# Optimization experiments

Measured on AMD Instinct MI355X. Metric: run time of the kernel, lower is better.

Reference implementation:

```python
import jax, jax.numpy as jnp
import numpy as np

B, S, D, H = 4, 2048, 2048, 16
HD = D // H  # 128
THETA = 10000.0


def setup_inputs() -> dict:
    key = jax.random.key(0)
    k1, k2, k3 = jax.random.split(key, 3)
    x = jax.random.normal(k1, (B, S, D), dtype=jnp.float32)
    wqkv = jax.random.normal(k2, (3 * D, D), dtype=jnp.float32) * (1.0 / np.sqrt(D))
    wo = jax.random.normal(k3, (D, D), dtype=jnp.float32) * (1.0 / np.sqrt(D))
    return {"x": x, "wqkv": wqkv, "wo": wo}


def _rotate_half(t):
    t1 = t[..., : t.shape[-1] // 2]
    t2 = t[..., t.shape[-1] // 2 :]
    return jnp.concatenate([-t2, t1], axis=-1)


def reference(x, wqkv, wo):
    b, s, d = x.shape
    h, hd = H, HD
    # fused QKV projection (Linear without bias: x @ W^T)
    qkv = jnp.einsum("bsd,ed->bse", x, wqkv).reshape(b, s, 3, h, hd)
    xq, xk, xv = qkv[:, :, 0], qkv[:, :, 1], qkv[:, :, 2]

    # RoPE tables (start_pos = 0)
    inv_freq = 1.0 / (THETA ** (jnp.arange(0, hd, 2, dtype=jnp.float32) / hd))
    t = jnp.arange(s, dtype=jnp.float32)
    freqs = jnp.outer(t, inv_freq)  # [s, hd/2]
    cos = jnp.concatenate([jnp.cos(freqs)] * 2, axis=-1).reshape(1, s, 1, hd)
    sin = jnp.concatenate([jnp.sin(freqs)] * 2, axis=-1).reshape(1, s, 1, hd)

    xq = xq * cos + _rotate_half(xq) * sin
    xk = xk * cos + _rotate_half(xk) * sin

    # causal SDPA (kv_cache is None, seq_len > 1)
    scale = 1.0 / np.sqrt(hd)
    scores = jnp.einsum("bqhd,bkhd->bhqk", xq, xk) * scale
    causal = jnp.tril(jnp.ones((s, s), dtype=bool))
    scores = jnp.where(causal, scores, jnp.finfo(scores.dtype).min)
    attn = jax.nn.softmax(scores, axis=-1)
    out = jnp.einsum("bhqk,bkhd->bqhd", attn, xv).reshape(b, s, d)
    return jnp.einsum("bsd,od->bso", out, wo)
```

## Files before the change

### kernel.cpp

```cpp
#include <hip/hip_runtime.h>

typedef unsigned short u16;
typedef unsigned int u32;
typedef __bf16 bf16x8 __attribute__((ext_vector_type(8)));
typedef float f32x4 __attribute__((ext_vector_type(4)));

#define S_LEN 2048
#define NH 16
#define HD 128

#define AS1 __attribute__((address_space(1)))
#define AS3 __attribute__((address_space(3)))

__device__ __forceinline__ u16 f2bf(float x) {
  u32 u = __builtin_bit_cast(u32, x);
  u32 r = u + 0x7FFFu + ((u >> 16) & 1u);
  return (u16)(r >> 16);
}
__device__ __forceinline__ float bf2f(u16 b) {
  return __builtin_bit_cast(float, (u32)b << 16);
}

__global__ void cvt_f32_bf16(const float* __restrict__ in, u16* __restrict__ out, int n4) {
  int i = blockIdx.x * 256 + threadIdx.x;
  if (i >= n4) return;
  float4 v = ((const float4*)in)[i];
  ushort4 o;
  o.x = f2bf(v.x); o.y = f2bf(v.y); o.z = f2bf(v.z); o.w = f2bf(v.w);
  ((ushort4*)out)[i] = o;
}

__global__ void build_tab(float* __restrict__ tab) {
  int t = blockIdx.x * 256 + threadIdx.x;
  int s = t >> 6, j = t & 63;
  float inv = exp2f(-(float)j * 0.20762050593045083f);
  float ang = (float)s * inv;
  tab[t] = cosf(ang);
  tab[131072 + t] = sinf(ang);
}

__device__ __forceinline__ void storeC(u16* p, float v) { *p = f2bf(v); }
__device__ __forceinline__ void storeC(float* p, float v) { *p = v; }

template <typename OutT>
__global__ __launch_bounds__(512, 2) void gemm_bt6(const u16* __restrict__ A, const u16* __restrict__ B,
                                                   OutT* __restrict__ C, int M, int N, int K, int nbx) {
  __shared__ alignas(16) u16 LDS[65536];
  char* lds = (char*)LDS;
  const int tid = threadIdx.x;
  const int lane = tid & 63;
  const int w = tid >> 6;
  const int wr = w >> 2, wc = w & 3;
  const int g = lane >> 4, c = lane & 15;

  const int nwg = gridDim.x;
  const int id = blockIdx.x;
  const int sw = (id & 7) * (nwg >> 3) + (id >> 3);
  const int bx = sw % nbx, by = sw / nbx;
  const size_t rowBase = (size_t)by * 256;
  const size_t colBase = (size_t)bx * 256;

  const int half = w & 1;
  const int sub = (w >> 1) & 3;
  const size_t ldb = (size_t)K * 2;
  const int srow = lane >> 3;
  const int soff = ((lane & 7) ^ srow) << 4;
  const char* ApS = (const char*)A + (rowBase + half * 128 + srow) * ldb + soff;
  const char* BpS = (const char*)B + (colBase + half * 128 + srow) * ldb + soff;

  auto stA = [&](int u, int blk) {
    const int r0 = blk * 32 + sub * 8;
    const int dst = ((u & 1) * 2 + half) * 16384 + r0 * 128;
    __builtin_amdgcn_global_load_lds((const AS1 void*)(ApS + (size_t)r0 * ldb + (size_t)u * 128),
                                     (AS3 void*)(lds + dst), 16, 0, 0);
  };
  auto stB = [&](int u, int jj) {
    const int r0 = (sub * 4 + jj) * 8;
    const int dst = 65536 + ((u & 1) * 2 + half) * 16384 + r0 * 128;
    __builtin_amdgcn_global_load_lds((const AS1 void*)(BpS + (size_t)r0 * ldb + (size_t)u * 128),
                                     (AS3 void*)(lds + dst), 16, 0, 0);
  };

  const int swz = (c & 7) << 4;
  auto rdA = [&](int bA, int mi, int kk) -> bf16x8 {
    return *(const bf16x8*)(lds + bA + mi * 2048 + c * 128 + ((kk * 64 + g * 16) ^ swz));
  };
  auto rdB = [&](int bB, int n, int kk) -> bf16x8 {
    return *(const bf16x8*)(lds + bB + n * 2048 + c * 128 + ((kk * 64 + g * 16) ^ swz));
  };

  f32x4 acc[8][4];
#pragma unroll
  for (int m = 0; m < 8; ++m)
#pragma unroll
    for (int n = 0; n < 4; ++n) acc[m][n] = f32x4{0.f, 0.f, 0.f, 0.f};

  bf16x8 bf_[4][2];
  bf16x8 aP[4], aQ[4];

  auto loadA = [&](bf16x8 (&s)[4], int bA, int mi) {
    s[0] = rdA(bA, mi, 0); s[1] = rdA(bA, mi, 1);
    s[2] = rdA(bA, mi + 1, 0); s[3] = rdA(bA, mi + 1, 1);
  };
  auto loadR1 = [&](int bA, int bB) {
    loadA(aP, bA, 0);
#pragma unroll
    for (int n = 0; n < 4; ++n) { bf_[n][0] = rdB(bB, n, 0); bf_[n][1] = rdB(bB, n, 1); }
  };
  auto MFMA2 = [&](int mi, bf16x8 (&s)[4]) {
#pragma unroll
    for (int n = 0; n < 4; ++n) {
      acc[mi][n]     = __builtin_amdgcn_mfma_f32_16x16x32_bf16(s[0], bf_[n][0], acc[mi][n], 0, 0, 0);
      acc[mi][n]     = __builtin_amdgcn_mfma_f32_16x16x32_bf16(s[1], bf_[n][1], acc[mi][n], 0, 0, 0);
      acc[mi + 1][n] = __builtin_amdgcn_mfma_f32_16x16x32_bf16(s[2], bf_[n][0], acc[mi + 1][n], 0, 0, 0);
      acc[mi + 1][n] = __builtin_amdgcn_mfma_f32_16x16x32_bf16(s[3], bf_[n][1], acc[mi + 1][n], 0, 0, 0);
    }
  };

  const int NT = K >> 6;

#pragma unroll
  for (int b = 0; b < 4; ++b) stA(0, b);
#pragma unroll
  for (int j = 0; j < 4; ++j) stB(0, j);
#pragma unroll
  for (int b = 0; b < 4; ++b) stA(1, b);
#pragma unroll
  for (int j = 0; j < 4; ++j) stB(1, j);
  asm volatile("s_waitcnt vmcnt(8)" ::: "memory");
  __builtin_amdgcn_s_barrier();
  {
    const int bA0 = wr * 16384;
    const int bB0 = 65536 + (wc >> 1) * 16384 + (wc & 1) * 8192;
    loadR1(bA0, bB0);
  }

#pragma unroll 1
  for (int t = 0; t < NT; ++t) {
    const int bA = (t & 1) * 32768 + wr * 16384;
    const int bB = 65536 + (t & 1) * 32768 + (wc >> 1) * 16384 + (wc & 1) * 8192;
    loadA(aQ, bA, 2);
    if (t >= 1 && t + 1 < NT) stA(t + 1, 3);
    asm volatile("s_waitcnt lgkmcnt(4)" ::: "memory");
    __builtin_amdgcn_sched_barrier(0);
    __builtin_amdgcn_s_setprio(1);
    MFMA2(0, aP);
    __builtin_amdgcn_s_setprio(0);
    __builtin_amdgcn_sched_barrier(0);
    __builtin_amdgcn_s_barrier();
    loadA(aP, bA, 4);
    if (t + 2 < NT) { stA(t + 2, 0); stB(t + 2, 0); stB(t + 2, 1); }
    asm volatile("s_waitcnt lgkmcnt(4)" ::: "memory");
    __builtin_amdgcn_sched_barrier(0);
    __builtin_amdgcn_s_setprio(1);
    MFMA2(2, aQ);
    __builtin_amdgcn_s_setprio(0);
    __builtin_amdgcn_sched_barrier(0);
    __builtin_amdgcn_s_barrier();
    loadA(aQ, bA, 6);
    if (t + 2 < NT) { stA(t + 2, 1); stB(t + 2, 2); stB(t + 2, 3); }
    asm volatile("s_waitcnt lgkmcnt(4)" ::: "memory");
    __builtin_amdgcn_sched_barrier(0);
    __builtin_amdgcn_s_setprio(1);
    MFMA2(4, aP);
    __builtin_amdgcn_s_setprio(0);
    __builtin_amdgcn_sched_barrier(0);
    __builtin_amdgcn_s_barrier();
    if (t + 2 < NT) stA(t + 2, 2);
    asm volatile("s_waitcnt lgkmcnt(0)" ::: "memory");
    __builtin_amdgcn_sched_barrier(0);
    __builtin_amdgcn_s_setprio(1);
    MFMA2(6, aQ);
    __builtin_amdgcn_s_setprio(0);
    __builtin_amdgcn_sched_barrier(0);
    if (t + 2 < NT) { asm volatile("s_waitcnt vmcnt(7)" ::: "memory"); }
    else            { asm volatile("s_waitcnt vmcnt(0)" ::: "memory"); }
    __builtin_amdgcn_s_barrier();
    if (t + 1 < NT) {
      const int bA1 = ((t + 1) & 1) * 32768 + wr * 16384;
      const int bB1 = 65536 + ((t + 1) & 1) * 32768 + (wc >> 1) * 16384 + (wc & 1) * 8192;
      loadR1(bA1, bB1);
    }
  }

#pragma unroll
  for (int m = 0; m < 8; ++m)
#pragma unroll
    for (int n = 0; n < 4; ++n) {
      size_t row = rowBase + wr * 128 + m * 16 + g * 4;
      size_t col = colBase + wc * 64 + n * 16 + c;
#pragma unroll
      for (int r = 0; r < 4; ++r)
        storeC(&C[(row + r) * (size_t)N + col], acc[m][n][r]);
    }
}

__global__ void rope_qk(const u16* __restrict__ qkv, const float* __restrict__ tab,
                        u16* __restrict__ Q, u16* __restrict__ K) {
  int idx = blockIdx.x * 256 + threadIdx.x;
  int j = idx & 63;
  int s = (idx >> 6) & (S_LEN - 1);
  int h = (idx >> 17) & (NH - 1);
  int b = idx >> 21;
  float cs = tab[s * 64 + j];
  float sn = tab[131072 + s * 64 + j];
  size_t qbase = (((size_t)(b * S_LEN + s) * 3 + 0) * NH + h) * HD;
  size_t kbase = qbase + (size_t)NH * HD;
  size_t o = ((size_t)(b * NH + h) * S_LEN + s) * HD;
  float q1 = bf2f(qkv[qbase + j]),  q2 = bf2f(qkv[qbase + j + 64]);
  Q[o + j]      = f2bf(q1 * cs - q2 * sn);
  Q[o + j + 64] = f2bf(q2 * cs + q1 * sn);
  float k1 = bf2f(qkv[kbase + j]), k2 = bf2f(qkv[kbase + j + 64]);
  K[o + j]      = f2bf(k1 * cs - k2 * sn);
  K[o + j + 64] = f2bf(k2 * cs + k1 * sn);
}

__global__ void v_transpose(const u16* __restrict__ qkv, u16* __restrict__ Vt) {
  __shared__ u16 t[32][33];
  int bh = blockIdx.z;
  int s0 = blockIdx.x * 32;
  int d0 = blockIdx.y * 32;
  int b = bh >> 4, h = bh & 15;
  int col = threadIdx.x & 31;
  int row = threadIdx.x >> 5;
#pragma unroll
  for (int i = 0; i < 4; ++i) {
    int s = row + i * 8;
    t[s][col] = qkv[(((size_t)(b * S_LEN + s0 + s) * 3 + 2) * NH + h) * HD + d0 + col];
  }
  __syncthreads();
  size_t vb = ((size_t)bh * HD + d0) * S_LEN + s0;
#pragma unroll
  for (int i = 0; i < 4; ++i) {
    int d = row + i * 8;
    Vt[vb + (size_t)d * S_LEN + col] = t[col][d];
  }
}

__global__ __launch_bounds__(512, 4) void attn_fwd(const u16* __restrict__ Q, const u16* __restrict__ K,
                                                   const u16* __restrict__ Vt, u16* __restrict__ O) {
  __shared__ alignas(16) u16 Ks[2 * 64 * 128];
  __shared__ alignas(16) u16 Vs[2 * 128 * 64];
  __shared__ alignas(16) u16 Pl[8 * 16 * 64];
  const int tid = threadIdx.x;
  const int lane = tid & 63;
  const int w = tid >> 6;
  const int g = lane >> 4, c = lane & 15;
  const int bh = blockIdx.x;
  const int pair = blockIdx.y;
  const int b = bh >> 4, h = bh & 15;

  const u16* Qb = Q + (size_t)bh * S_LEN * HD;
  const u16* Kb = K + (size_t)bh * S_LEN * HD;
  const u16* Vb = Vt + (size_t)bh * HD * S_LEN;
  const float SL = 0.12751753f;
  const int swz = (c & 7) << 4;

  int ldsOff[2], srcK[2], srcV[2];
#pragma unroll
  for (int ii = 0; ii < 2; ++ii) {
    int p = (w * 2 + ii) * 1024 + lane * 16;
    ldsOff[ii] = p;
    int rk = p >> 8, ik = p & 255;
    srcK[ii] = rk * 256 + (ik ^ ((rk & 7) << 4));
    int rv = p >> 7, iv = p & 127;
    srcV[ii] = rv * (S_LEN * 2) + (iv ^ ((rv & 7) << 4));
  }
  int koff[4], voff[2];
#pragma unroll
  for (int kb = 0; kb < 4; ++kb) koff[kb] = (kb * 64 + g * 16) ^ swz;
  voff[0] = (g * 16) ^ swz;
  voff[1] = (64 + g * 16) ^ swz;
  int poff[4];
#pragma unroll
  for (int t = 0; t < 4; ++t) poff[t] = (t * 32 + g * 8) ^ swz;
  char* Pw = (char*)Pl + w * 2048;

#pragma unroll 1
  for (int ph = 0; ph < 2; ++ph) {
    const int sti = ph ? (15 - pair) : pair;
    const int qb0 = sti * 128;
    const int q0 = qb0 + w * 16;

    bf16x8 qf[4];
#pragma unroll
    for (int kb = 0; kb < 4; ++kb)
      qf[kb] = *(const bf16x8*)&Qb[(size_t)(q0 + c) * HD + kb * 32 + g * 8];

    f32x4 acc[8];
#pragma unroll
    for (int cb = 0; cb < 8; ++cb) acc[cb] = f32x4{0.f, 0.f, 0.f, 0.f};
    float m_i = -3e38f, l_i = 0.f;

    const int nsteps = sti * 2 + 2;
#pragma unroll
    for (int ii = 0; ii < 2; ++ii) {
      __builtin_amdgcn_global_load_lds((const AS1 void*)((const char*)Kb + srcK[ii]),
                                       (AS3 void*)((char*)Ks + ldsOff[ii] - lane * 16), 16, 0, 0);
      __builtin_amdgcn_global_load_lds((const AS1 void*)((const char*)Vb + srcV[ii]),
                                       (AS3 void*)((char*)Vs + ldsOff[ii] - lane * 16), 16, 0, 0);
    }
    __syncthreads();
    int cur = 0;

#pragma unroll 1
    for (int st = 0; st < nsteps; ++st) {
      const int kv0 = st << 6;
      if (st + 1 < nsteps) {
        const char* kbase = (const char*)Kb + (size_t)(kv0 + 64) * 256;
        const char* vbase = (const char*)Vb + (size_t)(kv0 + 64) * 2;
        const int nb = (cur ^ 1) * 16384;
#pragma unroll
        for (int ii = 0; ii < 2; ++ii) {
          __builtin_amdgcn_global_load_lds((const AS1 void*)(kbase + srcK[ii]),
                                           (AS3 void*)((char*)Ks + nb + ldsOff[ii] - lane * 16), 16, 0, 0);
          __builtin_amdgcn_global_load_lds((const AS1 void*)(vbase + srcV[ii]),
                                           (AS3 void*)((char*)Vs + nb + ldsOff[ii] - lane * 16), 16, 0, 0);
        }
      }
      if (kv0 < q0 + 16) {
        const char* Kt = (const char*)Ks + cur * 16384;
        const char* Vtl = (const char*)Vs + cur * 16384;
        f32x4 s[4];
#pragma unroll
        for (int t = 0; t < 4; ++t) s[t] = f32x4{0.f, 0.f, 0.f, 0.f};
#pragma unroll
        for (int t = 0; t < 4; ++t)
#pragma unroll
          for (int kb = 0; kb < 4; ++kb) {
            bf16x8 kf = *(const bf16x8*)(Kt + t * 4096 + c * 256 + koff[kb]);
            s[t] = __builtin_amdgcn_mfma_f32_16x16x32_bf16(kf, qf[kb], s[t], 0, 0, 0);
          }
        if (kv0 + 63 > q0) {
          const int lim = q0 + c - kv0 - 4 * g;
#pragma unroll
          for (int t = 0; t < 4; ++t)
#pragma unroll
            for (int r = 0; r < 4; ++r)
              s[t][r] = (16 * t + r <= lim) ? s[t][r] : -3e38f;
        }
        float mx = s[0][0];
#pragma unroll
        for (int t = 0; t < 4; ++t)
#pragma unroll
          for (int r = 0; r < 4; ++r) mx = fmaxf(mx, s[t][r]);
        mx = fmaxf(mx, __shfl_xor(mx, 16));
        mx = fmaxf(mx, __shfl_xor(mx, 32));
        const float mn = fmaxf(m_i, mx);
        const float alpha = exp2f((m_i - mn) * SL);
        float rs = 0.f;
#pragma unroll
        for (int t = 0; t < 4; ++t) {
          float p0 = exp2f((s[t][0] - mn) * SL);
          float p1 = exp2f((s[t][1] - mn) * SL);
          float p2 = exp2f((s[t][2] - mn) * SL);
          float p3 = exp2f((s[t][3] - mn) * SL);
          rs += (p0 + p1) + (p2 + p3);
          ushort4 pw;
          pw.x = f2bf(p0); pw.y = f2bf(p1); pw.z = f2bf(p2); pw.w = f2bf(p3);
          *(ushort4*)(Pw + c * 128 + poff[t]) = pw;
        }
        rs += __shfl_xor(rs, 16);
        rs += __shfl_xor(rs, 32);
        l_i = l_i * alpha + rs;
        m_i = mn;
        float ar[4];
#pragma unroll
        for (int r = 0; r < 4; ++r) ar[r] = __shfl(alpha, 4 * g + r);
#pragma unroll
        for (int cb = 0; cb < 8; ++cb)
#pragma unroll
          for (int r = 0; r < 4; ++r) acc[cb][r] *= ar[r];
        bf16x8 pa0 = *(const bf16x8*)(Pw + c * 128 + voff[0]);
        bf16x8 pa1 = *(const bf16x8*)(Pw + c * 128 + voff[1]);
#pragma unroll
        for (int cb = 0; cb < 8; ++cb) {
          bf16x8 vf0 = *(const bf16x8*)(Vtl + cb * 2048 + c * 128 + voff[0]);
          acc[cb] = __builtin_amdgcn_mfma_f32_16x16x32_bf16(pa0, vf0, acc[cb], 0, 0, 0);
          bf16x8 vf1 = *(const bf16x8*)(Vtl + cb * 2048 + c * 128 + voff[1]);
          acc[cb] = __builtin_amdgcn_mfma_f32_16x16x32_bf16(pa1, vf1, acc[cb], 0, 0, 0);
        }
      }
      __syncthreads();
      cur ^= 1;
    }
    float linv = 1.0f / l_i;
    float lr[4];
#pragma unroll
    for (int r = 0; r < 4; ++r) lr[r] = __shfl(linv, 4 * g + r);
#pragma unroll
    for (int cb = 0; cb < 8; ++cb)
#pragma unroll
      for (int r = 0; r < 4; ++r) {
        int q = q0 + 4 * g + r;
        O[(((size_t)b * S_LEN + q) * NH + h) * HD + cb * 16 + c] = f2bf(acc[cb][r] * lr[r]);
      }
  }
}

extern "C" void kernel_launch(void* const* d_in, const int* in_sizes, int n_in,
                              void* d_out, int out_size, void* d_ws, size_t ws_size,
                              hipStream_t stream) {
  const float* x    = (const float*)d_in[0];
  const float* wqkv = (const float*)d_in[1];
  const float* wo   = (const float*)d_in[2];
  float* out = (float*)d_out;
  char* ws = (char*)d_ws;

  u16*  xb    = (u16*)(ws + 0);
  u16*  wqkvb = (u16*)(ws + 33554432);
  float* tab  = (float*)(ws + 58720256);
  u16*  wob   = (u16*)(ws + 58720256);
  u16*  qkvb  = (u16*)(ws + 67108864);
  u16*  Vt    = (u16*)(ws + 167772160);
  u16*  attn  = (u16*)(ws + 0);
  u16*  Qr = (u16*)d_out;
  u16*  Kr = (u16*)d_out + 16777216;

  cvt_f32_bf16<<<16384, 256, 0, stream>>>(x, xb, 16777216 / 4);
  cvt_f32_bf16<<<12288, 256, 0, stream>>>(wqkv, wqkvb, 12582912 / 4);
  build_tab<<<512, 256, 0, stream>>>(tab);

  gemm_bt6<u16><<<768, 512, 0, stream>>>(xb, wqkvb, qkvb, 8192, 6144, 2048, 24);

  rope_qk<<<32768, 256, 0, stream>>>(qkvb, tab, Qr, Kr);
  v_transpose<<<dim3(64, 4, 64), 256, 0, stream>>>(qkvb, Vt);

  cvt_f32_bf16<<<4096, 256, 0, stream>>>(wo, wob, 4194304 / 4);

  attn_fwd<<<dim3(64, 8), 512, 0, stream>>>(Qr, Kr, Vt, attn);

  gemm_bt6<float><<<256, 512, 0, stream>>>(attn, wob, out, 8192, 2048, 2048, 8);
}
```

Measured before the change: 434.2 us.

## Fuse RoPE and V transpose into the QKV GEMM epilogue

The QKV projection GEMM now writes its outputs directly. For Q and K tiles it applies RoPE in registers and writes to head-major buffers. For V tiles it transposes through LDS and writes Vt. This removes the bf16 qkv intermediate and the separate rope_qk and v_transpose kernels, along with their global memory round trips. To make it work, the B-operand row mapping changes so each wave holds matching d and d+64 columns. The cost is a heavier epilogue with scattered 2-byte stores for Q and K and extra table loads.

```diff
diff --git a/kernel.cpp b/kernel.cpp
--- a/kernel.cpp
+++ b/kernel.cpp
@@ -3,6 +3,7 @@
 typedef unsigned short u16;
 typedef unsigned int u32;
 typedef __bf16 bf16x8 __attribute__((ext_vector_type(8)));
+typedef unsigned short u16x8 __attribute__((ext_vector_type(8)));
 typedef float f32x4 __attribute__((ext_vector_type(4)));
 
 #define S_LEN 2048
@@ -42,9 +43,12 @@
 __device__ __forceinline__ void storeC(u16* p, float v) { *p = f2bf(v); }
 __device__ __forceinline__ void storeC(float* p, float v) { *p = v; }
 
-template <typename OutT>
-__global__ __launch_bounds__(512, 2) void gemm_bt6(const u16* __restrict__ A, const u16* __restrict__ B,
-                                                   OutT* __restrict__ C, int M, int N, int K, int nbx) {
+template <int EPI, typename OutT>
+__global__ __launch_bounds__(512, 2) void gemm_fused(const u16* __restrict__ A, const u16* __restrict__ B,
+                                                     OutT* __restrict__ C, const float* __restrict__ tab,
+                                                     u16* __restrict__ Qr, u16* __restrict__ Kr,
+                                                     u16* __restrict__ Vt,
+                                                     int M, int N, int K, int nbx) {
   __shared__ alignas(16) u16 LDS[65536];
   char* lds = (char*)LDS;
   const int tid = threadIdx.x;
@@ -81,12 +85,16 @@
                                      (AS3 void*)(lds + dst), 16, 0, 0);
   };
 
+  const int dq32 = (wc & 1) * 32;
   const int swz = (c & 7) << 4;
   auto rdA = [&](int bA, int mi, int kk) -> bf16x8 {
     return *(const bf16x8*)(lds + bA + mi * 2048 + c * 128 + ((kk * 64 + g * 16) ^ swz));
   };
   auto rdB = [&](int bB, int n, int kk) -> bf16x8 {
-    return *(const bf16x8*)(lds + bB + n * 2048 + c * 128 + ((kk * 64 + g * 16) ^ swz));
+    int row_l;
+    if (EPI) row_l = dq32 + (n & 1) * 16 + ((n >= 2) ? 64 : 0) + c;
+    else     row_l = (wc & 1) * 64 + n * 16 + c;
+    return *(const bf16x8*)(lds + bB + row_l * 128 + ((kk * 64 + g * 16) ^ swz));
   };
 
   f32x4 acc[8][4];
@@ -131,14 +139,14 @@
   __builtin_amdgcn_s_barrier();
   {
     const int bA0 = wr * 16384;
-    const int bB0 = 65536 + (wc >> 1) * 16384 + (wc & 1) * 8192;
+    const int bB0 = 65536 + (wc >> 1) * 16384;
     loadR1(bA0, bB0);
   }
 
 #pragma unroll 1
   for (int t = 0; t < NT; ++t) {
     const int bA = (t & 1) * 32768 + wr * 16384;
-    const int bB = 65536 + (t & 1) * 32768 + (wc >> 1) * 16384 + (wc & 1) * 8192;
+    const int bB = 65536 + (t & 1) * 32768 + (wc >> 1) * 16384;
     loadA(aQ, bA, 2);
     if (t >= 1 && t + 1 < NT) stA(t + 1, 3);
     asm volatile("s_waitcnt lgkmcnt(4)" ::: "memory");
@@ -178,62 +186,68 @@
     __builtin_amdgcn_s_barrier();
     if (t + 1 < NT) {
       const int bA1 = ((t + 1) & 1) * 32768 + wr * 16384;
-      const int bB1 = 65536 + ((t + 1) & 1) * 32768 + (wc >> 1) * 16384 + (wc & 1) * 8192;
+      const int bB1 = 65536 + ((t + 1) & 1) * 32768 + (wc >> 1) * 16384;
       loadR1(bA1, bB1);
     }
   }
 
-#pragma unroll
-  for (int m = 0; m < 8; ++m)
-#pragma unroll
-    for (int n = 0; n < 4; ++n) {
-      size_t row = rowBase + wr * 128 + m * 16 + g * 4;
-      size_t col = colBase + wc * 64 + n * 16 + c;
-#pragma unroll
-      for (int r = 0; r < 4; ++r)
-        storeC(&C[(row + r) * (size_t)N + col], acc[m][n][r]);
+  if (EPI == 0) {
+#pragma unroll
+    for (int m = 0; m < 8; ++m)
+#pragma unroll
+      for (int n = 0; n < 4; ++n) {
+        size_t row = rowBase + wr * 128 + m * 16 + g * 4;
+        size_t col = colBase + wc * 64 + n * 16 + c;
+#pragma unroll
+        for (int r = 0; r < 4; ++r)
+          storeC(&C[(row + r) * (size_t)N + col], acc[m][n][r]);
+      }
+  } else {
+    const int slot = (int)(colBase >> 11);
+    const int h = (((int)colBase >> 7) & 15) + (wc >> 1);
+    const int bidx = (int)(rowBase >> 11);
+    const int sbase = ((int)rowBase & 2047) + wr * 128;
+
+    if (slot < 2) {
+      u16* dst = (slot == 0 ? Qr : Kr) + (size_t)(bidx * NH + h) * S_LEN * HD;
+#pragma unroll
+      for (int m = 0; m < 8; ++m)
+#pragma unroll
+        for (int r = 0; r < 4; ++r) {
+          const int s = sbase + m * 16 + g * 4 + r;
+          u16* drow = dst + (size_t)s * HD;
+          const float* tc = tab + s * 64;
+          const float* ts = tab + 131072 + s * 64;
+#pragma unroll
+          for (int n = 0; n < 2; ++n) {
+            const int dlo = dq32 + n * 16 + c;
+            float cs = tc[dlo], sn = ts[dlo];
+            float xlo = acc[m][n][r], xhi = acc[m][n + 2][r];
+            drow[dlo]      = f2bf(cs * xlo - sn * xhi);
+            drow[dlo + 64] = f2bf(cs * xhi + sn * xlo);
+          }
+        }
+    } else {
+      char* lv = lds + w * 16384;
+#pragma unroll
+      for (int m = 0; m < 8; ++m)
+#pragma unroll
+        for (int n = 0; n < 4; ++n) {
+          const int ld = ((n >= 2) ? 32 : 0) + (n & 1) * 16 + c;
+          ushort4 pk;
+          pk.x = f2bf(acc[m][n][0]); pk.y = f2bf(acc[m][n][1]);
+          pk.z = f2bf(acc[m][n][2]); pk.w = f2bf(acc[m][n][3]);
+          *(ushort4*)(lv + ld * 256 + ((m * 32 + g * 8) ^ ((ld & 7) << 4))) = pk;
+        }
+      u16* vbase = Vt + (size_t)(bidx * NH + h) * HD * S_LEN;
+#pragma unroll
+      for (int rr = 0; rr < 16; ++rr) {
+        const int ld = rr * 4 + (lane >> 4);
+        const int d = dq32 + ld + ((rr >= 8) ? 32 : 0);
+        u16x8 v = *(const u16x8*)(lv + ld * 256 + (((lane & 15) * 16) ^ ((ld & 7) << 4)));
+        *(u16x8*)(vbase + (size_t)d * S_LEN + sbase + (lane & 15) * 8) = v;
+      }
     }
-}
-
-__global__ void rope_qk(const u16* __restrict__ qkv, const float* __restrict__ tab,
-                        u16* __restrict__ Q, u16* __restrict__ K) {
-  int idx = blockIdx.x * 256 + threadIdx.x;
-  int j = idx & 63;
-  int s = (idx >> 6) & (S_LEN - 1);
-  int h = (idx >> 17) & (NH - 1);
-  int b = idx >> 21;
-  float cs = tab[s * 64 + j];
-  float sn = tab[131072 + s * 64 + j];
-  size_t qbase = (((size_t)(b * S_LEN + s) * 3 + 0) * NH + h) * HD;
-  size_t kbase = qbase + (size_t)NH * HD;
-  size_t o = ((size_t)(b * NH + h) * S_LEN + s) * HD;
-  float q1 = bf2f(qkv[qbase + j]),  q2 = bf2f(qkv[qbase + j + 64]);
-  Q[o + j]      = f2bf(q1 * cs - q2 * sn);
-  Q[o + j + 64] = f2bf(q2 * cs + q1 * sn);
-  float k1 = bf2f(qkv[kbase + j]), k2 = bf2f(qkv[kbase + j + 64]);
-  K[o + j]      = f2bf(k1 * cs - k2 * sn);
-  K[o + j + 64] = f2bf(k2 * cs + k1 * sn);
-}
-
-__global__ void v_transpose(const u16* __restrict__ qkv, u16* __restrict__ Vt) {
-  __shared__ u16 t[32][33];
-  int bh = blockIdx.z;
-  int s0 = blockIdx.x * 32;
-  int d0 = blockIdx.y * 32;
-  int b = bh >> 4, h = bh & 15;
-  int col = threadIdx.x & 31;
-  int row = threadIdx.x >> 5;
-#pragma unroll
-  for (int i = 0; i < 4; ++i) {
-    int s = row + i * 8;
-    t[s][col] = qkv[(((size_t)(b * S_LEN + s0 + s) * 3 + 2) * NH + h) * HD + d0 + col];
-  }
-  __syncthreads();
-  size_t vb = ((size_t)bh * HD + d0) * S_LEN + s0;
-#pragma unroll
-  for (int i = 0; i < 4; ++i) {
-    int d = row + i * 8;
-    Vt[vb + (size_t)d * S_LEN + col] = t[col][d];
   }
 }
 
@@ -411,7 +425,6 @@
   u16*  wqkvb = (u16*)(ws + 33554432);
   float* tab  = (float*)(ws + 58720256);
   u16*  wob   = (u16*)(ws + 58720256);
-  u16*  qkvb  = (u16*)(ws + 67108864);
   u16*  Vt    = (u16*)(ws + 167772160);
   u16*  attn  = (u16*)(ws + 0);
   u16*  Qr = (u16*)d_out;
@@ -421,14 +434,13 @@
   cvt_f32_bf16<<<12288, 256, 0, stream>>>(wqkv, wqkvb, 12582912 / 4);
   build_tab<<<512, 256, 0, stream>>>(tab);
 
-  gemm_bt6<u16><<<768, 512, 0, stream>>>(xb, wqkvb, qkvb, 8192, 6144, 2048, 24);
-
-  rope_qk<<<32768, 256, 0, stream>>>(qkvb, tab, Qr, Kr);
-  v_transpose<<<dim3(64, 4, 64), 256, 0, stream>>>(qkvb, Vt);
+  gemm_fused<1, u16><<<768, 512, 0, stream>>>(xb, wqkvb, (u16*)nullptr, tab, Qr, Kr, Vt,
+                                              8192, 6144, 2048, 24);
 
   cvt_f32_bf16<<<4096, 256, 0, stream>>>(wo, wob, 4194304 / 4);
 
   attn_fwd<<<dim3(64, 8), 512, 0, stream>>>(Qr, Kr, Vt, attn);
 
-  gemm_bt6<float><<<256, 512, 0, stream>>>(attn, wob, out, 8192, 2048, 2048, 8);
-}
+  gemm_fused<0, float><<<256, 512, 0, stream>>>(attn, wob, out, nullptr, nullptr, nullptr, nullptr,
+                                                8192, 2048, 2048, 8);
+}
```

Result: faster. 406.0 us (-6.5%).
